# Optimization experiments

Hardware: AMD Instinct MI355X
Metric: run time of the kernel (lower is better)

Reference implementation:

```python
import jax, jax.numpy as jnp
import numpy as np

B, Q, K, DQ, DK = 4, 256, 1024, 256, 256


def setup_inputs() -> dict:
    key = jax.random.key(0)
    ks = jax.random.split(key, 7)
    q = jax.random.normal(ks[0], (B, Q, DQ), dtype=jnp.float32)
    k = jax.random.normal(ks[1], (B, K, DK), dtype=jnp.float32)
    v = jax.random.normal(ks[2], (B, K, DK), dtype=jnp.float32)
    mask = jax.random.randint(ks[3], (B, K), 0, 2).astype(bool)
    # torch Linear(in,out,bias=False): y = x @ W.T ; store as [in,out] for einsum
    Wq = jax.random.normal(ks[4], (DQ, DK), dtype=jnp.float32) / np.sqrt(DQ)
    Wk = jax.random.normal(ks[5], (DK, DK), dtype=jnp.float32) / np.sqrt(DK)
    wv = jax.random.normal(ks[6], (DK,), dtype=jnp.float32) / np.sqrt(DK)
    return {"q": q, "k": k, "v": v, "mask": mask, "Wq": Wq, "Wk": Wk, "wv": wv}


def reference(q, k, v, mask, Wq, Wk, wv):
    # Additive (Bahdanau) attention. Original redundantly projects repeated
    # copies; projecting once then broadcasting is the same math.
    qp = jnp.einsum('bqd,de->bqe', q, Wq)          # [B,Q,DK]
    kp = jnp.einsum('bkd,de->bke', k, Wk)          # [B,K,DK]
    h = jnp.tanh(qp[:, :, None, :] + kp[:, None, :, :])  # [B,Q,K,DK]
    scores = jnp.einsum('bqke,e->bqk', h, wv)      # [B,Q,K]
    scores = jnp.where(mask[:, None, :], scores, -jnp.inf)
    probs = jax.nn.softmax(scores, axis=-1)        # [B,Q,K]
    attended = jnp.einsum('bqk,bkd->bqd', probs, v)
    return attended
```

## Files before the change

kernel.cpp:

```cpp
#include <hip/hip_runtime.h>
#include <hip/hip_bf16.h>

#define B_ 4
#define Q_ 256
#define K_ 1024
#define D_ 256
#define NVPAD 768
#define LOG2E 1.44269504f

__device__ __forceinline__ float fexp2(float x) {
    float r; asm("v_exp_f32 %0, %1" : "=v"(r) : "v"(x)); return r;
}
__device__ __forceinline__ float frcp(float x) {
    float r; asm("v_rcp_f32 %0, %1" : "=v"(r) : "v"(x)); return r;
}

__global__ void compact_kernel(const int* __restrict__ mask,
                               ushort* __restrict__ kidx,
                               short* __restrict__ slot_of,
                               int* __restrict__ nvalid) {
    const int b = blockIdx.x, lane = threadIdx.x;
    const int* m = mask + b * K_;
    const int base = lane * 16;
    int cnt = 0;
#pragma unroll
    for (int i = 0; i < 16; ++i) cnt += (m[base + i] != 0);
    int inc = cnt;
#pragma unroll
    for (int d = 1; d < 64; d <<= 1) {
        int tt = __shfl_up(inc, d);
        if (lane >= d) inc += tt;
    }
    const int total = __shfl(inc, 63);
    int pos = inc - cnt;
    ushort* kb = kidx + b * K_;
    short* so  = slot_of + b * K_;
    for (int i = 0; i < 16; ++i) {
        int kk = base + i;
        if (m[kk] != 0) { kb[pos] = (ushort)kk; so[kk] = (short)pos; ++pos; }
        else so[kk] = -1;
    }
    for (int j = total + lane; j < K_; j += 64) kb[j] = 0;
    if (lane == 0) nvalid[b] = total;
}

__global__ __launch_bounds__(256) void proj_kernel(const float* __restrict__ q,
                                                   const float* __restrict__ k,
                                                   const float* __restrict__ Wq,
                                                   const float* __restrict__ Wk,
                                                   const short* __restrict__ slot_of,
                                                   float* __restrict__ qpE,
                                                   float* __restrict__ kpC,
                                                   float scale) {
    const int t = threadIdx.x;
    const bool isQ = blockIdx.x < 16;
    const float* A; const float* W; int m0;
    if (isQ) { A = q; W = Wq; m0 = blockIdx.x * 64; }
    else     { A = k; W = Wk; m0 = (blockIdx.x - 16) * 64; }

    __shared__ float As[16][65];
    __shared__ float Ws[16][64];
    __shared__ short s_slot[64];
    if (!isQ && t < 64) s_slot[t] = slot_of[m0 + t];

    const int tx = t & 15, ty = t >> 4;
    const int n0 = blockIdx.y * 64;
    const int ar = t >> 2, ac = (t & 3) * 4;
    const int wr = t >> 4, wc = (t & 15) * 4;
    float c[4][4] = {};
    for (int kb = 0; kb < 256; kb += 16) {
        __syncthreads();
        float4 av = *(const float4*)(A + (size_t)(m0 + ar) * 256 + kb + ac);
        As[ac + 0][ar] = av.x; As[ac + 1][ar] = av.y;
        As[ac + 2][ar] = av.z; As[ac + 3][ar] = av.w;
        float4 wvv = *(const float4*)(W + (size_t)(kb + wr) * 256 + n0 + wc);
        wvv.x *= scale; wvv.y *= scale; wvv.z *= scale; wvv.w *= scale;
        *(float4*)(&Ws[wr][wc]) = wvv;
        __syncthreads();
#pragma unroll
        for (int kk = 0; kk < 16; ++kk) {
            float4 bv = *(const float4*)(&Ws[kk][tx * 4]);
#pragma unroll
            for (int i = 0; i < 4; ++i) {
                float a = As[kk][ty * 4 + i];
                c[i][0] = fmaf(a, bv.x, c[i][0]);
                c[i][1] = fmaf(a, bv.y, c[i][1]);
                c[i][2] = fmaf(a, bv.z, c[i][2]);
                c[i][3] = fmaf(a, bv.w, c[i][3]);
            }
        }
    }
    if (isQ) {
#pragma unroll
        for (int i = 0; i < 4; ++i) {
            float4 o = make_float4(fexp2(c[i][0]), fexp2(c[i][1]),
                                   fexp2(c[i][2]), fexp2(c[i][3]));
            *(float4*)(qpE + (size_t)(m0 + ty * 4 + i) * 256 + n0 + tx * 4) = o;
        }
    } else {
        const int b = m0 >> 10;
        float* kpCb = kpC + (size_t)b * 64 * NVPAD * 4;
        const int e4 = (n0 + tx * 4) >> 2;
#pragma unroll
        for (int i = 0; i < 4; ++i) {
            const int sl = s_slot[ty * 4 + i];
            if (sl >= 0) {
                float4 o = make_float4(fexp2(c[i][0]), fexp2(c[i][1]),
                                       fexp2(c[i][2]), fexp2(c[i][3]));
                *(float4*)(kpCb + ((size_t)e4 * NVPAD + sl) * 4) = o;
            }
        }
    }
}

__global__ __launch_bounds__(1024, 2) void attn_kernel(const float* __restrict__ qpE,
                                                       const float* __restrict__ kpC,
                                                       const float* __restrict__ v,
                                                       const ushort* __restrict__ kidx_g,
                                                       const int* __restrict__ nvalid_g,
                                                       const float* __restrict__ wv,
                                                       float* __restrict__ out) {
    __shared__ float  s_sc[2][1024];
    __shared__ ushort s_kidx[1024];
    __shared__ float4 s_pv[32][64];
    __shared__ float  s_inv[2];

    const int tid  = threadIdx.x;
    const int lane = tid & 63;
    const int wave = tid >> 6;
    const int sl8  = lane & 7;
    const int ec   = lane >> 3;

    int bid = blockIdx.x;
    bid = (bid & 7) * 64 + (bid >> 3);
    const int b  = bid >> 7;
    const int qi = bid & 127;
    const int q0 = qi * 2;
    const int nv = nvalid_g[b];
    const int iters = (nv + 127) >> 7;

    s_kidx[tid] = (tid < nv) ? kidx_g[b * K_ + tid] : (ushort)0;
    ((float2*)s_sc)[tid] = make_float2(0.f, 0.f);
    __syncthreads();

    const float4* Bp  = (const float4*)kpC + (size_t)b * 64 * NVPAD;
    const float*  A0g = qpE + ((size_t)(b * Q_ + q0) << 8);
    const float*  A1g = A0g + 256;

    for (int eq = 0; eq < 4; ++eq) {
        const int e0 = eq * 64 + ec * 8;
        float A0[8], A1[8], W[8];
        {
            float4 x0 = *(const float4*)(A0g + e0);
            float4 x1 = *(const float4*)(A0g + e0 + 4);
            A0[0]=x0.x; A0[1]=x0.y; A0[2]=x0.z; A0[3]=x0.w;
            A0[4]=x1.x; A0[5]=x1.y; A0[6]=x1.z; A0[7]=x1.w;
            float4 y0 = *(const float4*)(A1g + e0);
            float4 y1 = *(const float4*)(A1g + e0 + 4);
            A1[0]=y0.x; A1[1]=y0.y; A1[2]=y0.z; A1[3]=y0.w;
            A1[4]=y1.x; A1[5]=y1.y; A1[6]=y1.z; A1[7]=y1.w;
            float4 w0 = *(const float4*)(wv + e0);
            float4 w1 = *(const float4*)(wv + e0 + 4);
            W[0]=w0.x; W[1]=w0.y; W[2]=w0.z; W[3]=w0.w;
            W[4]=w1.x; W[5]=w1.y; W[6]=w1.z; W[7]=w1.w;
        }
        const float4* BpE = Bp + (size_t)(eq * 16 + ec * 2) * NVPAD;

#pragma unroll 2
        for (int i = 0; i < iters; ++i) {
            const int s = i * 128 + wave * 8 + sl8;
            float4 B0 = BpE[s];
            float4 B1 = BpE[NVPAD + s];
            float a0 = 0.f, a1 = 0.f;
            a0 = fmaf(W[0], frcp(fmaf(A0[0], B0.x, 1.f)), a0);
            a1 = fmaf(W[0], frcp(fmaf(A1[0], B0.x, 1.f)), a1);
            a0 = fmaf(W[1], frcp(fmaf(A0[1], B0.y, 1.f)), a0);
            a1 = fmaf(W[1], frcp(fmaf(A1[1], B0.y, 1.f)), a1);
            a0 = fmaf(W[2], frcp(fmaf(A0[2], B0.z, 1.f)), a0);
            a1 = fmaf(W[2], frcp(fmaf(A1[2], B0.z, 1.f)), a1);
            a0 = fmaf(W[3], frcp(fmaf(A0[3], B0.w, 1.f)), a0);
            a1 = fmaf(W[3], frcp(fmaf(A1[3], B0.w, 1.f)), a1);
            a0 = fmaf(W[4], frcp(fmaf(A0[4], B1.x, 1.f)), a0);
            a1 = fmaf(W[4], frcp(fmaf(A1[4], B1.x, 1.f)), a1);
            a0 = fmaf(W[5], frcp(fmaf(A0[5], B1.y, 1.f)), a0);
            a1 = fmaf(W[5], frcp(fmaf(A1[5], B1.y, 1.f)), a1);
            a0 = fmaf(W[6], frcp(fmaf(A0[6], B1.z, 1.f)), a0);
            a1 = fmaf(W[6], frcp(fmaf(A1[6], B1.z, 1.f)), a1);
            a0 = fmaf(W[7], frcp(fmaf(A0[7], B1.w, 1.f)), a0);
            a1 = fmaf(W[7], frcp(fmaf(A1[7], B1.w, 1.f)), a1);
            a0 += __shfl_xor(a0, 8);  a1 += __shfl_xor(a1, 8);
            a0 += __shfl_xor(a0, 16); a1 += __shfl_xor(a1, 16);
            a0 += __shfl_xor(a0, 32); a1 += __shfl_xor(a1, 32);
            if (ec == 0 && s < nv) {
                s_sc[0][s] += a0;
                s_sc[1][s] += a1;
            }
        }
    }
    __syncthreads();

    if (wave < 2) {
        const int qq = wave;
        float mx = -3.0e38f;
        for (int j = lane; j < nv; j += 64) mx = fmaxf(mx, -2.f * s_sc[qq][j]);
#pragma unroll
        for (int off = 32; off > 0; off >>= 1) mx = fmaxf(mx, __shfl_xor(mx, off));
        float sum = 0.f;
        for (int j = lane; j < nv; j += 64) {
            float e = fexp2((-2.f * s_sc[qq][j] - mx) * LOG2E);
            s_sc[qq][j] = e;
            sum += e;
        }
#pragma unroll
        for (int off = 32; off > 0; off >>= 1) sum += __shfl_xor(sum, off);
        if (lane == 0) s_inv[qq] = frcp(sum);
    }
    __syncthreads();

    {
        const int dl = tid & 63;
        const int kq = tid >> 6;
        float4 o0 = {0, 0, 0, 0}, o1 = {0, 0, 0, 0};
        const float4* v4 = (const float4*)(v + ((size_t)b * K_ << 8));
        for (int k = kq; k < nv; k += 16) {
            int vr = s_kidx[k];
            float4 vv = v4[((size_t)vr << 6) + dl];
            float p0 = s_sc[0][k], p1 = s_sc[1][k];
            o0.x = fmaf(p0, vv.x, o0.x); o0.y = fmaf(p0, vv.y, o0.y);
            o0.z = fmaf(p0, vv.z, o0.z); o0.w = fmaf(p0, vv.w, o0.w);
            o1.x = fmaf(p1, vv.x, o1.x); o1.y = fmaf(p1, vv.y, o1.y);
            o1.z = fmaf(p1, vv.z, o1.z); o1.w = fmaf(p1, vv.w, o1.w);
        }
        s_pv[kq * 2 + 0][dl] = o0;
        s_pv[kq * 2 + 1][dl] = o1;
        __syncthreads();
        if (tid < 128) {
            const int qq = tid >> 6, c = tid & 63;
            float4 s = {0, 0, 0, 0};
#pragma unroll
            for (int g = 0; g < 16; ++g) {
                float4 x = s_pv[g * 2 + qq][c];
                s.x += x.x; s.y += x.y; s.z += x.z; s.w += x.w;
            }
            const float inv = s_inv[qq];
            s.x *= inv; s.y *= inv; s.z *= inv; s.w *= inv;
            ((float4*)out)[((size_t)(b * Q_ + q0 + qq) << 6) + c] = s;
        }
    }
}

extern "C" void kernel_launch(void* const* d_in, const int* in_sizes, int n_in,
                              void* d_out, int out_size, void* d_ws, size_t ws_size,
                              hipStream_t stream) {
    const float* q    = (const float*)d_in[0];
    const float* k    = (const float*)d_in[1];
    const float* v    = (const float*)d_in[2];
    const int*   mask = (const int*)d_in[3];
    const float* Wq   = (const float*)d_in[4];
    const float* Wk   = (const float*)d_in[5];
    const float* wv   = (const float*)d_in[6];
    float* out = (float*)d_out;

    float* qpE    = (float*)d_ws;
    float* kpC    = qpE + (size_t)B_ * Q_ * D_;
    ushort* kidx  = (ushort*)(kpC + (size_t)B_ * 64 * NVPAD * 4);
    short* slot_of = (short*)(kidx + (size_t)B_ * K_);
    int* nvalid   = (int*)(slot_of + (size_t)B_ * K_);

    const float c2 = 2.885390082f;

    compact_kernel<<<dim3(B_), 64, 0, stream>>>(mask, kidx, slot_of, nvalid);
    proj_kernel<<<dim3(80, 4), 256, 0, stream>>>(q, k, Wq, Wk, slot_of, qpE, kpC, c2);
    attn_kernel<<<dim3(512), 1024, 0, stream>>>(qpE, kpC, v, kidx, nvalid, wv, out);
}
```

Baseline: 65.27 us.

## Share one reciprocal across two query rows and widen projection blocks to 512 threads

In the attention score loop, two reciprocals 1/u and 1/v are replaced by a single reciprocal of u*v, with each term recovered by multiplying by the other factor. This halves the transcendental (v_rcp) count per element in exchange for a few extra multiplies and a somewhat higher risk of overflow or precision loss when u*v gets large. Separately, the projection kernel now runs 512 threads per block, each computing a 2x4 tile instead of 4x4. Tile loads are split so half the threads load the A tile and half load the W tile. This aims for more parallelism and less work per thread in that small GEMM.

New measurement: 77.24 us. 1.18x slower.

```diff
diff --git a/kernel.cpp b/kernel.cpp
--- a/kernel.cpp
+++ b/kernel.cpp
@@ -44,7 +44,7 @@
     if (lane == 0) nvalid[b] = total;
 }
 
-__global__ __launch_bounds__(256) void proj_kernel(const float* __restrict__ q,
+__global__ __launch_bounds__(512) void proj_kernel(const float* __restrict__ q,
                                                    const float* __restrict__ k,
                                                    const float* __restrict__ Wq,
                                                    const float* __restrict__ Wk,
@@ -58,52 +58,58 @@
     if (isQ) { A = q; W = Wq; m0 = blockIdx.x * 64; }
     else     { A = k; W = Wk; m0 = (blockIdx.x - 16) * 64; }
 
-    __shared__ float As[16][65];
+    __shared__ float As[16][66];
     __shared__ float Ws[16][64];
     __shared__ short s_slot[64];
     if (!isQ && t < 64) s_slot[t] = slot_of[m0 + t];
 
-    const int tx = t & 15, ty = t >> 4;
+    const int tx = t & 15;
+    const int my = t >> 4;
     const int n0 = blockIdx.y * 64;
-    const int ar = t >> 2, ac = (t & 3) * 4;
-    const int wr = t >> 4, wc = (t & 15) * 4;
-    float c[4][4] = {};
+    float c[2][4] = {};
     for (int kb = 0; kb < 256; kb += 16) {
         __syncthreads();
-        float4 av = *(const float4*)(A + (size_t)(m0 + ar) * 256 + kb + ac);
-        As[ac + 0][ar] = av.x; As[ac + 1][ar] = av.y;
-        As[ac + 2][ar] = av.z; As[ac + 3][ar] = av.w;
-        float4 wvv = *(const float4*)(W + (size_t)(kb + wr) * 256 + n0 + wc);
-        wvv.x *= scale; wvv.y *= scale; wvv.z *= scale; wvv.w *= scale;
-        *(float4*)(&Ws[wr][wc]) = wvv;
+        if (t < 256) {
+            const int ar = t >> 2, ac = (t & 3) * 4;
+            float4 av = *(const float4*)(A + (size_t)(m0 + ar) * 256 + kb + ac);
+            As[ac + 0][ar] = av.x; As[ac + 1][ar] = av.y;
+            As[ac + 2][ar] = av.z; As[ac + 3][ar] = av.w;
+        } else {
+            const int t2 = t - 256;
+            const int wr = t2 >> 4, wc = (t2 & 15) * 4;
+            float4 wvv = *(const float4*)(W + (size_t)(kb + wr) * 256 + n0 + wc);
+            wvv.x *= scale; wvv.y *= scale; wvv.z *= scale; wvv.w *= scale;
+            *(float4*)(&Ws[wr][wc]) = wvv;
+        }
         __syncthreads();
 #pragma unroll
         for (int kk = 0; kk < 16; ++kk) {
+            float2 aa = *(const float2*)(&As[kk][my * 2]);
             float4 bv = *(const float4*)(&Ws[kk][tx * 4]);
-#pragma unroll
-            for (int i = 0; i < 4; ++i) {
-                float a = As[kk][ty * 4 + i];
-                c[i][0] = fmaf(a, bv.x, c[i][0]);
-                c[i][1] = fmaf(a, bv.y, c[i][1]);
-                c[i][2] = fmaf(a, bv.z, c[i][2]);
-                c[i][3] = fmaf(a, bv.w, c[i][3]);
-            }
+            c[0][0] = fmaf(aa.x, bv.x, c[0][0]);
+            c[0][1] = fmaf(aa.x, bv.y, c[0][1]);
+            c[0][2] = fmaf(aa.x, bv.z, c[0][2]);
+            c[0][3] = fmaf(aa.x, bv.w, c[0][3]);
+            c[1][0] = fmaf(aa.y, bv.x, c[1][0]);
+            c[1][1] = fmaf(aa.y, bv.y, c[1][1]);
+            c[1][2] = fmaf(aa.y, bv.z, c[1][2]);
+            c[1][3] = fmaf(aa.y, bv.w, c[1][3]);
         }
     }
     if (isQ) {
 #pragma unroll
-        for (int i = 0; i < 4; ++i) {
+        for (int i = 0; i < 2; ++i) {
             float4 o = make_float4(fexp2(c[i][0]), fexp2(c[i][1]),
                                    fexp2(c[i][2]), fexp2(c[i][3]));
-            *(float4*)(qpE + (size_t)(m0 + ty * 4 + i) * 256 + n0 + tx * 4) = o;
+            *(float4*)(qpE + (size_t)(m0 + my * 2 + i) * 256 + n0 + tx * 4) = o;
         }
     } else {
         const int b = m0 >> 10;
         float* kpCb = kpC + (size_t)b * 64 * NVPAD * 4;
         const int e4 = (n0 + tx * 4) >> 2;
 #pragma unroll
-        for (int i = 0; i < 4; ++i) {
-            const int sl = s_slot[ty * 4 + i];
+        for (int i = 0; i < 2; ++i) {
+            const int sl = s_slot[my * 2 + i];
             if (sl >= 0) {
                 float4 o = make_float4(fexp2(c[i][0]), fexp2(c[i][1]),
                                        fexp2(c[i][2]), fexp2(c[i][3]));
@@ -172,22 +178,24 @@
             float4 B0 = BpE[s];
             float4 B1 = BpE[NVPAD + s];
             float a0 = 0.f, a1 = 0.f;
-            a0 = fmaf(W[0], frcp(fmaf(A0[0], B0.x, 1.f)), a0);
-            a1 = fmaf(W[0], frcp(fmaf(A1[0], B0.x, 1.f)), a1);
-            a0 = fmaf(W[1], frcp(fmaf(A0[1], B0.y, 1.f)), a0);
-            a1 = fmaf(W[1], frcp(fmaf(A1[1], B0.y, 1.f)), a1);
-            a0 = fmaf(W[2], frcp(fmaf(A0[2], B0.z, 1.f)), a0);
-            a1 = fmaf(W[2], frcp(fmaf(A1[2], B0.z, 1.f)), a1);
-            a0 = fmaf(W[3], frcp(fmaf(A0[3], B0.w, 1.f)), a0);
-            a1 = fmaf(W[3], frcp(fmaf(A1[3], B0.w, 1.f)), a1);
-            a0 = fmaf(W[4], frcp(fmaf(A0[4], B1.x, 1.f)), a0);
-            a1 = fmaf(W[4], frcp(fmaf(A1[4], B1.x, 1.f)), a1);
-            a0 = fmaf(W[5], frcp(fmaf(A0[5], B1.y, 1.f)), a0);
-            a1 = fmaf(W[5], frcp(fmaf(A1[5], B1.y, 1.f)), a1);
-            a0 = fmaf(W[6], frcp(fmaf(A0[6], B1.z, 1.f)), a0);
-            a1 = fmaf(W[6], frcp(fmaf(A1[6], B1.z, 1.f)), a1);
-            a0 = fmaf(W[7], frcp(fmaf(A0[7], B1.w, 1.f)), a0);
-            a1 = fmaf(W[7], frcp(fmaf(A1[7], B1.w, 1.f)), a1);
+#define SIGP(Ae0, Ae1, We, Bv)                                              \
+            {                                                               \
+                float u  = fmaf(Ae0, Bv, 1.f);                              \
+                float vv = fmaf(Ae1, Bv, 1.f);                              \
+                float r  = frcp(u * vv);                                    \
+                float tt = We * r;                                          \
+                a0 = fmaf(tt, vv, a0);                                      \
+                a1 = fmaf(tt, u, a1);                                       \
+            }
+            SIGP(A0[0], A1[0], W[0], B0.x)
+            SIGP(A0[1], A1[1], W[1], B0.y)
+            SIGP(A0[2], A1[2], W[2], B0.z)
+            SIGP(A0[3], A1[3], W[3], B0.w)
+            SIGP(A0[4], A1[4], W[4], B1.x)
+            SIGP(A0[5], A1[5], W[5], B1.y)
+            SIGP(A0[6], A1[6], W[6], B1.z)
+            SIGP(A0[7], A1[7], W[7], B1.w)
+#undef SIGP
             a0 += __shfl_xor(a0, 8);  a1 += __shfl_xor(a1, 8);
             a0 += __shfl_xor(a0, 16); a1 += __shfl_xor(a1, 16);
             a0 += __shfl_xor(a0, 32); a1 += __shfl_xor(a1, 32);
@@ -270,6 +278,6 @@
     const float c2 = 2.885390082f;
 
     compact_kernel<<<dim3(B_), 64, 0, stream>>>(mask, kidx, slot_of, nvalid);
-    proj_kernel<<<dim3(80, 4), 256, 0, stream>>>(q, k, Wq, Wk, slot_of, qpE, kpC, c2);
+    proj_kernel<<<dim3(80, 4), 512, 0, stream>>>(q, k, Wq, Wk, slot_of, qpE, kpC, c2);
     attn_kernel<<<dim3(512), 1024, 0, stream>>>(qpE, kpC, v, kidx, nvalid, wv, out);
 }
```
